# Kernel tuning notes

Measured on AMD Instinct MI355X. Metric: run time of the kernel, lower is better.

Reference implementation:

```python
import jax, jax.numpy as jnp
import numpy as np

B, S, D, HID, H, VOCAB, DFF = 4, 2048, 512, 512, 8, 32000, 2048
DK = HID // H   # per-head Q/K dim
DV = D // H     # per-head V dim


def sinusoidal_pe(L, d):
    pos = jnp.arange(L, dtype=jnp.float32)[:, None]
    i = jnp.arange(d, dtype=jnp.float32)[None, :]
    ang = pos / jnp.power(jnp.float32(10000.0), i / d)
    return jnp.where(jnp.arange(d)[None, :] % 2 == 0, jnp.sin(ang), jnp.cos(ang))  # [L, d]


def layer_norm(x, gamma, beta, eps=1e-5):
    mu = jnp.mean(x, axis=-1, keepdims=True)
    var = jnp.mean((x - mu) ** 2, axis=-1, keepdims=True)
    return (x - mu) * jax.lax.rsqrt(var + eps) * gamma + beta


def setup_inputs() -> dict:
    key = jax.random.key(0)
    ks = jax.random.split(key, 24)
    n = lambda k, shape, fan: jax.random.normal(k, shape, dtype=jnp.float32) / np.sqrt(fan)
    inp = {
        'x': jax.random.randint(ks[0], (B, S), 0, VOCAB),
        'emb': n(ks[1], (VOCAB, D), D),
        'WfQ': n(ks[2], (D, HID), D), 'bfQ': jnp.zeros((HID,), jnp.float32),
        'WfK': n(ks[3], (D, HID), D), 'bfK': jnp.zeros((HID,), jnp.float32),
        'WfV': n(ks[4], (D, D), D),   'bfV': jnp.zeros((D,), jnp.float32),
        'WQ': n(ks[5], (H, HID, DK), HID), 'bQ': jnp.zeros((H, DK), jnp.float32),
        'WK': n(ks[6], (H, HID, DK), HID), 'bK': jnp.zeros((H, DK), jnp.float32),
        'WV': n(ks[7], (H, D, DV), D),     'bV': jnp.zeros((H, DV), jnp.float32),
        'Wo': n(ks[8], (D, D), D),   'bo': jnp.zeros((D,), jnp.float32),
        'W1': n(ks[9], (D, DFF), D), 'b1': jnp.zeros((DFF,), jnp.float32),
        'W2': n(ks[10], (DFF, D), DFF), 'b2': jnp.zeros((D,), jnp.float32),
        'gamma': jnp.ones((D,), jnp.float32), 'beta': jnp.zeros((D,), jnp.float32),
    }
    return inp


def reference(x, emb, WfQ, bfQ, WfK, bfK, WfV, bfV, WQ, bQ, WK, bK, WV, bV,
              Wo, bo, W1, b1, W2, b2, gamma, beta):
    z = emb[x] + sinusoidal_pe(x.shape[1], D)[None]            # [B,S,D]
    Q = z @ WfQ + bfQ                                           # [B,S,HID]
    K = z @ WfK + bfK
    V = z @ WfV + bfV                                           # [B,S,D]
    # per-head projections (batched equivalent of the per-head Linear loop)
    Qh = jnp.einsum('bsd,hdk->bhsk', Q, WQ) + bQ[None, :, None, :]  # [B,H,S,DK]
    Kh = jnp.einsum('bsd,hdk->bhsk', K, WK) + bK[None, :, None, :]
    Vh = jnp.einsum('bsd,hdv->bhsv', V, WV) + bV[None, :, None, :]  # [B,H,S,DV]
    scores = jnp.einsum('bhqk,bhsk->bhqs', Qh, Kh) / np.sqrt(DK)    # [B,H,S,S]
    attn = jax.nn.softmax(scores, axis=-1)
    heads = jnp.einsum('bhqs,bhsv->bhqv', attn, Vh)                 # [B,H,S,DV]
    concat = heads.transpose(0, 2, 1, 3).reshape(x.shape[0], x.shape[1], D)
    attn_out = concat @ Wo + bo
    a = layer_norm(attn_out + z, gamma, beta)
    ffn = jax.nn.relu(a @ W1 + b1) @ W2 + b2
    out = layer_norm(ffn + a, gamma, beta)   # same (shared) LayerNorm params, as in source
    return jax.nn.relu(out)
```

## Files before the change

### kernel.cpp

```cpp
#include <hip/hip_runtime.h>
#include <math.h>

typedef __bf16 bf16;
typedef __bf16 bf16x8 __attribute__((ext_vector_type(8)));
typedef __bf16 bf16x4 __attribute__((ext_vector_type(4)));
typedef _Float16 f16;
typedef _Float16 f16x8 __attribute__((ext_vector_type(8)));
typedef _Float16 f16x4 __attribute__((ext_vector_type(4)));
typedef _Float16 f16x2 __attribute__((ext_vector_type(2)));
typedef __fp16 h16x2 __attribute__((ext_vector_type(2)));
typedef float f32x4 __attribute__((ext_vector_type(4)));
typedef unsigned int u32;

#define S_LEN 2048
#define QSCALE 0.18033688011112042f

#if __has_builtin(__builtin_amdgcn_exp2f)
#define EXP2(x) __builtin_amdgcn_exp2f(x)
#else
#define EXP2(x) exp2f(x)
#endif

__device__ __forceinline__ void gload_lds16(const void* g, void* l) {
  __builtin_amdgcn_global_load_lds((const __attribute__((address_space(1))) u32*)g,
                                   (__attribute__((address_space(3))) u32*)l, 16, 0, 0);
}

__global__ __launch_bounds__(256) void embed_pe(const int* __restrict__ x,
    const float* __restrict__ emb, bf16* __restrict__ zb)
{
  const int row = blockIdx.x;
  const int s = row & (S_LEN - 1);
  const int tok = x[row];
  const float* e = emb + (size_t)tok * 512;
  bf16* zbr = zb + (size_t)row * 512;
  for (int i = threadIdx.x; i < 512; i += 256) {
    float invf = __expf((float)i * (-9.210340371976184f / 512.0f));
    float ang = (float)s * invf;
    float pe = (i & 1) ? __cosf(ang) : __sinf(ang);
    zbr[i] = (bf16)(e[i] + pe);
  }
}

__global__ __launch_bounds__(256) void conv_t(
    const float* __restrict__ Wo, const float* __restrict__ W1, const float* __restrict__ W2,
    const float* __restrict__ WQ, const float* __restrict__ WK, const float* __restrict__ WV,
    const float* __restrict__ WfQ, const float* __restrict__ WfK, const float* __restrict__ WfV,
    bf16* __restrict__ wot, bf16* __restrict__ w1t, bf16* __restrict__ w2t,
    bf16* __restrict__ wqt, bf16* __restrict__ wkt, bf16* __restrict__ wvt,
    bf16* __restrict__ wfqp, bf16* __restrict__ wfkp, bf16* __restrict__ wfvp)
{
  __shared__ float T[64][65];
  const int y = blockIdx.y, x = blockIdx.x;
  if (y >= 6) {
    int g = x * 256 + threadIdx.x;
    const float* in = y == 6 ? WfQ : (y == 7 ? WfK : WfV);
    bf16* outp = y == 6 ? wfqp : (y == 7 ? wfkp : wfvp);
    float4 v = *(const float4*)(in + (size_t)g * 4);
    bf16x4 o = {(bf16)v.x, (bf16)v.y, (bf16)v.z, (bf16)v.w};
    *(bf16x4*)(outp + (size_t)g * 4) = o;
    return;
  }
  const int tx = threadIdx.x & 63, ty = threadIdx.x >> 6;
  const float* src; bf16* dst;
  int src_cols, dst_cols; float scale = 1.f;
  if (y == 0) {
    if (x >= 64) return;
    int kt = x & 7, nt = x >> 3;
    src = Wo + (size_t)(kt * 64) * 512 + nt * 64; src_cols = 512;
    dst = wot + (size_t)(nt * 64) * 512 + kt * 64; dst_cols = 512;
  } else if (y == 1) {
    int kt = x & 7, nt = x >> 3;
    src = W1 + (size_t)(kt * 64) * 2048 + nt * 64; src_cols = 2048;
    dst = w1t + (size_t)(nt * 64) * 512 + kt * 64; dst_cols = 512;
  } else if (y == 2) {
    int kt = x & 31, nt = x >> 5;
    src = W2 + (size_t)(kt * 64) * 512 + nt * 64; src_cols = 512;
    dst = w2t + (size_t)(nt * 64) * 2048 + kt * 64; dst_cols = 2048;
  } else {
    if (x >= 64) return;
    const float* W = y == 3 ? WQ : (y == 4 ? WK : WV);
    bf16* o = y == 3 ? wqt : (y == 4 ? wkt : wvt);
    if (y == 3) scale = QSCALE;
    int h = x >> 3, rt = x & 7;
    src = W + (size_t)(h * 512 + rt * 64) * 64; src_cols = 64;
    dst = o + (size_t)(h * 64) * 512 + rt * 64; dst_cols = 512;
  }
  #pragma unroll
  for (int i = 0; i < 16; i++) {
    int rr = i * 4 + ty;
    T[rr][tx] = src[(size_t)rr * src_cols + tx];
  }
  __syncthreads();
  #pragma unroll
  for (int i = 0; i < 16; i++) {
    int rr = i * 4 + ty;
    dst[(size_t)rr * dst_cols + tx] = (bf16)(T[tx][rr] * scale);
  }
}

__global__ __launch_bounds__(256) void bias_comb(
    const float* __restrict__ bfQ, const float* __restrict__ bfK, const float* __restrict__ bfV,
    const float* __restrict__ WQ, const float* __restrict__ WK, const float* __restrict__ WV,
    const float* __restrict__ bQ, const float* __restrict__ bK, const float* __restrict__ bV,
    float* __restrict__ bc)
{
  int n = blockIdx.x * 4 + (threadIdx.x >> 6);
  int lane = threadIdx.x & 63;
  int z = n >> 9, hk = n & 511, h = hk >> 6, k = hk & 63;
  const float* bf = z == 0 ? bfQ : (z == 1 ? bfK : bfV);
  const float* W  = z == 0 ? WQ  : (z == 1 ? WK  : WV);
  const float* bH = z == 0 ? bQ  : (z == 1 ? bK  : bV);
  float s = 0.f;
  for (int e = lane; e < 512; e += 64)
    s += bf[e] * W[((size_t)h * 512 + e) * 64 + k];
  #pragma unroll
  for (int m = 1; m < 64; m <<= 1) s += __shfl_xor(s, m, 64);
  if (lane == 0) {
    float v = s + bH[h * 64 + k];
    if (z == 0) v *= QSCALE;
    bc[n] = v;
  }
}

__global__ __launch_bounds__(256) void gemm_comb(
    const bf16* __restrict__ wqt, const bf16* __restrict__ wkt, const bf16* __restrict__ wvt,
    const bf16* __restrict__ wfqp, const bf16* __restrict__ wfkp, const bf16* __restrict__ wfvp,
    bf16* __restrict__ wc)
{
  __shared__ bf16 As[128 * 32];
  __shared__ bf16 Bs[64 * 32];
  const int z = blockIdx.z;
  const bf16* A  = z == 0 ? wqt : (z == 1 ? wkt : wvt);
  const bf16* Bt = z == 0 ? wfqp : (z == 1 ? wfkp : wfvp);
  bf16* outb = wc + (size_t)z * 262144;
  const int tid = threadIdx.x;
  const int wave = tid >> 6, lane = tid & 63, quad = lane >> 4, l16 = lane & 15;
  const int row0 = blockIdx.x * 128, col0 = blockIdx.y * 64;
  const int wm = wave >> 1, wn = wave & 1;
  f32x4 acc[4][2] = {};

  for (int kk = 0; kk < 512; kk += 32) {
    __syncthreads();
    #pragma unroll
    for (int r = 0; r < 2; r++) {
      int c = r * 256 + tid;
      gload_lds16(A + (size_t)(row0 + (c >> 2)) * 512 + kk + (c & 3) * 8, As + c * 8);
    }
    gload_lds16(Bt + (size_t)(col0 + (tid >> 2)) * 512 + kk + (tid & 3) * 8, Bs + tid * 8);
    __syncthreads();
    bf16x8 af[4], bfr[2];
    #pragma unroll
    for (int i = 0; i < 4; i++)
      af[i] = *(const bf16x8*)(As + (wm * 64 + i * 16 + l16) * 32 + quad * 8);
    #pragma unroll
    for (int i = 0; i < 2; i++)
      bfr[i] = *(const bf16x8*)(Bs + (wn * 32 + i * 16 + l16) * 32 + quad * 8);
    #pragma unroll
    for (int mt = 0; mt < 4; mt++)
      #pragma unroll
      for (int nt = 0; nt < 2; nt++)
        acc[mt][nt] = __builtin_amdgcn_mfma_f32_16x16x32_bf16(af[mt], bfr[nt], acc[mt][nt], 0, 0, 0);
  }
  #pragma unroll
  for (int nt = 0; nt < 2; nt++) {
    int col = col0 + wn * 32 + nt * 16 + l16;
    #pragma unroll
    for (int mt = 0; mt < 4; mt++) {
      int rowb = row0 + wm * 64 + mt * 16 + quad * 4;
      #pragma unroll
      for (int i = 0; i < 4; i++)
        outb[(size_t)(rowb + i) * 512 + col] = (bf16)acc[mt][nt][i];
    }
  }
}

#define GEMM_CORE(A_, Bt_, K_, KK0_, ITERS_)                                            \
  bf16x8 ar0, ar1, br0, br1;                                                            \
  const int c0 = tid, c1 = 256 + tid;                                                   \
  const size_t aoff0 = (size_t)(row0 + (c0 >> 2)) * (K_) + (c0 & 3) * 8;                \
  const size_t aoff1 = (size_t)(row0 + (c1 >> 2)) * (K_) + (c1 & 3) * 8;                \
  const size_t boff0 = (size_t)(col0 + (c0 >> 2)) * (K_) + (c0 & 3) * 8;                \
  const size_t boff1 = (size_t)(col0 + (c1 >> 2)) * (K_) + (c1 & 3) * 8;                \
  ar0 = *(const bf16x8*)((A_) + aoff0 + (KK0_));                                        \
  ar1 = *(const bf16x8*)((A_) + aoff1 + (KK0_));                                        \
  br0 = *(const bf16x8*)((Bt_) + boff0 + (KK0_));                                       \
  br1 = *(const bf16x8*)((Bt_) + boff1 + (KK0_));                                       \
  for (int it = 0; it < (ITERS_); it++) {                                               \
    bf16* AsB = As[it & 1];                                                             \
    bf16* BsB = Bs[it & 1];                                                             \
    *(bf16x8*)(AsB + c0 * 8) = ar0;                                                     \
    *(bf16x8*)(AsB + c1 * 8) = ar1;                                                     \
    *(bf16x8*)(BsB + c0 * 8) = br0;                                                     \
    *(bf16x8*)(BsB + c1 * 8) = br1;                                                     \
    __syncthreads();                                                                    \
    if (it + 1 < (ITERS_)) {                                                            \
      int kk = (KK0_) + (it + 1) * 32;                                                  \
      ar0 = *(const bf16x8*)((A_) + aoff0 + kk);                                        \
      ar1 = *(const bf16x8*)((A_) + aoff1 + kk);                                        \
      br0 = *(const bf16x8*)((Bt_) + boff0 + kk);                                      \
      br1 = *(const bf16x8*)((Bt_) + boff1 + kk);                                      \
    }                                                                                   \
    bf16x8 af[4], bfr[4];                                                               \
    _Pragma("unroll")                                                                   \
    for (int i = 0; i < 4; i++)                                                         \
      af[i] = *(const bf16x8*)(AsB + (wm * 64 + i * 16 + l16) * 32 + quad * 8);         \
    _Pragma("unroll")                                                                   \
    for (int i = 0; i < 4; i++)                                                         \
      bfr[i] = *(const bf16x8*)(BsB + (wn * 64 + i * 16 + l16) * 32 + quad * 8);        \
    _Pragma("unroll")                                                                   \
    for (int mt = 0; mt < 4; mt++)                                                      \
      _Pragma("unroll")                                                                 \
      for (int nt = 0; nt < 4; nt++)                                                    \
        acc[mt][nt] = __builtin_amdgcn_mfma_f32_16x16x32_bf16(af[mt], bfr[nt], acc[mt][nt], 0, 0, 0); \
  }

__global__ __launch_bounds__(256) void gemm_bt(
    const bf16* __restrict__ A, const bf16* __restrict__ Bt,
    const float* __restrict__ bias, bf16* __restrict__ outb,
    int M, int N, int K, int relu)
{
  __shared__ bf16 As[2][4096];
  __shared__ bf16 Bs[2][4096];
  const int tid = threadIdx.x;
  const int wave = tid >> 6, lane = tid & 63, quad = lane >> 4, l16 = lane & 15;
  const int row0 = blockIdx.x * 128, col0 = blockIdx.y * 128;
  const int wm = wave >> 1, wn = wave & 1;
  f32x4 acc[4][4] = {};
  GEMM_CORE(A, Bt, K, 0, K / 32)

  #pragma unroll
  for (int nt = 0; nt < 4; nt++) {
    int col = col0 + wn * 64 + nt * 16 + l16;
    float bv = bias[col];
    #pragma unroll
    for (int mt = 0; mt < 4; mt++) {
      int rowb = row0 + wm * 64 + mt * 16 + quad * 4;
      #pragma unroll
      for (int i = 0; i < 4; i++) {
        float v = acc[mt][nt][i] + bv;
        if (relu) v = fmaxf(v, 0.f);
        outb[(size_t)(rowb + i) * N + col] = (bf16)v;
      }
    }
  }
}

__global__ __launch_bounds__(256) void gemm_qkv(
    const bf16* __restrict__ A, const bf16* __restrict__ Bt,
    const float* __restrict__ bias, f16* __restrict__ qk, f16* __restrict__ Vt)
{
  __shared__ bf16 As[2][4096];
  __shared__ bf16 Bs[2][4096];
  const int tid = threadIdx.x;
  const int wave = tid >> 6, lane = tid & 63, quad = lane >> 4, l16 = lane & 15;
  const int row0 = blockIdx.x * 128, col0 = blockIdx.y * 128;
  const int wm = wave >> 1, wn = wave & 1;
  f32x4 acc[4][4] = {};
  GEMM_CORE(A, Bt, 512, 0, 16)

  #pragma unroll
  for (int nt = 0; nt < 4; nt++) {
    int col = col0 + wn * 64 + nt * 16 + l16;
    float bv = bias[col];
    if (col < 1024) {
      #pragma unroll
      for (int mt = 0; mt < 4; mt++) {
        int rowb = row0 + wm * 64 + mt * 16 + quad * 4;
        #pragma unroll
        for (int i = 0; i < 4; i++)
          qk[(size_t)(rowb + i) * 1024 + col] = (f16)(acc[mt][nt][i] + bv);
      }
    } else {
      int h = (col - 1024) >> 6, dv = col & 63;
      #pragma unroll
      for (int mt = 0; mt < 4; mt++) {
        int rowb = row0 + wm * 64 + mt * 16 + quad * 4;
        int b = rowb >> 11, s = rowb & 2047;
        f16x4 vv;
        #pragma unroll
        for (int i = 0; i < 4; i++) vv[i] = (f16)(acc[mt][nt][i] + bv);
        *(f16x4*)(Vt + ((size_t)((b * 8 + h) * 64 + dv)) * 2048 + s) = vv;
      }
    }
  }
}

__global__ __launch_bounds__(256) void gemm_part(
    const bf16* __restrict__ A, const bf16* __restrict__ Bt,
    bf16* __restrict__ Pa, bf16* __restrict__ Pb, int N, int K, int Kh)
{
  __shared__ bf16 As[2][4096];
  __shared__ bf16 Bs[2][4096];
  const int tid = threadIdx.x;
  const int wave = tid >> 6, lane = tid & 63, quad = lane >> 4, l16 = lane & 15;
  const int row0 = blockIdx.x * 128, col0 = blockIdx.y * 128;
  const int wm = wave >> 1, wn = wave & 1;
  const int kk0 = blockIdx.z * Kh;
  bf16* P = blockIdx.z ? Pb : Pa;
  f32x4 acc[4][4] = {};
  GEMM_CORE(A, Bt, K, kk0, Kh / 32)

  #pragma unroll
  for (int nt = 0; nt < 4; nt++) {
    int col = col0 + wn * 64 + nt * 16 + l16;
    #pragma unroll
    for (int mt = 0; mt < 4; mt++) {
      int rowb = row0 + wm * 64 + mt * 16 + quad * 4;
      #pragma unroll
      for (int i = 0; i < 4; i++)
        P[(size_t)(rowb + i) * N + col] = (bf16)acc[mt][nt][i];
    }
  }
}

__global__ __launch_bounds__(256, 2) void flash_attn(
    const f16* __restrict__ qk, const f16* __restrict__ Vt,
    bf16* __restrict__ Op, float* __restrict__ Rp)
{
  __shared__ f16 Ks[2][4096];
  __shared__ f16 Vs[2][4096];
  const int bh = blockIdx.y, b = bh >> 3, h = bh & 7;
  const int q0 = blockIdx.x * 128;
  const int quarter = blockIdx.z;
  const int tid = threadIdx.x;
  const int wave = tid >> 6, lane = tid & 63, quad = lane >> 4, l16 = lane & 15;

  const f16* Qb = qk + ((size_t)b * S_LEN) * 1024 + h * 64;
  const f16* Kb = Qb + 512;
  const f16* Vtb = Vt + ((size_t)bh * 64) * 2048;
  const int key0 = quarter * 512;

  f16x8 qf[2][2];
  #pragma unroll
  for (int f = 0; f < 2; f++) {
    int qrow = q0 + wave * 32 + f * 16 + l16;
    #pragma unroll
    for (int kh = 0; kh < 2; kh++)
      qf[f][kh] = *(const f16x8*)(Qb + (size_t)qrow * 1024 + kh * 32 + quad * 8);
  }

  f32x4 O[2][4] = {};
  f32x4 Osum[2] = {};
  const f16x4 onesA = {(f16)1.f, (f16)1.f, (f16)1.f, (f16)1.f};
  const int swz = l16 & 7;

  f16x8 kreg[2], vreg[2];
  const int srow = tid >> 3, soff = tid & 7;
  const int srow1 = srow + 32;

  {
    int kb = key0;
    kreg[0] = *(const f16x8*)(Kb + (size_t)(kb + srow) * 1024 + soff * 8);
    vreg[0] = *(const f16x8*)(Vtb + (size_t)srow * 2048 + kb + soff * 8);
    kreg[1] = *(const f16x8*)(Kb + (size_t)(kb + srow1) * 1024 + soff * 8);
    vreg[1] = *(const f16x8*)(Vtb + (size_t)srow1 * 2048 + kb + soff * 8);
  }

  for (int c = 0; c < 8; c++) {
    f16* KsB = Ks[c & 1];
    f16* VsB = Vs[c & 1];
    *(f16x8*)(KsB + srow * 64 + ((soff ^ (srow & 7)) * 8)) = kreg[0];
    *(f16x8*)(VsB + srow * 64 + ((soff ^ (srow & 7)) * 8)) = vreg[0];
    *(f16x8*)(KsB + srow1 * 64 + ((soff ^ (srow1 & 7)) * 8)) = kreg[1];
    *(f16x8*)(VsB + srow1 * 64 + ((soff ^ (srow1 & 7)) * 8)) = vreg[1];
    __syncthreads();
    if (c < 7) {
      int kb = key0 + (c + 1) * 64;
      kreg[0] = *(const f16x8*)(Kb + (size_t)(kb + srow) * 1024 + soff * 8);
      vreg[0] = *(const f16x8*)(Vtb + (size_t)srow * 2048 + kb + soff * 8);
      kreg[1] = *(const f16x8*)(Kb + (size_t)(kb + srow1) * 1024 + soff * 8);
      vreg[1] = *(const f16x8*)(Vtb + (size_t)srow1 * 2048 + kb + soff * 8);
    }

    #pragma unroll
    for (int nt = 0; nt < 4; nt++) {
      const f16* kp = KsB + (nt * 16 + l16) * 64;
      f16x8 kf0 = *(const f16x8*)(kp + ((quad ^ swz) * 8));
      f16x8 kf1 = *(const f16x8*)(kp + (((4 + quad) ^ swz) * 8));
      f16x4 pf[2];
      f32x4 a0 = {}, a1 = {};
      __builtin_amdgcn_s_setprio(1);
      a0 = __builtin_amdgcn_mfma_f32_16x16x32_f16(kf0, qf[0][0], a0, 0, 0, 0);
      a0 = __builtin_amdgcn_mfma_f32_16x16x32_f16(kf1, qf[0][1], a0, 0, 0, 0);
      a1 = __builtin_amdgcn_mfma_f32_16x16x32_f16(kf0, qf[1][0], a1, 0, 0, 0);
      a1 = __builtin_amdgcn_mfma_f32_16x16x32_f16(kf1, qf[1][1], a1, 0, 0, 0);
      __builtin_amdgcn_s_setprio(0);
      #pragma unroll
      for (int f = 0; f < 2; f++) {
        const f32x4& a = f == 0 ? a0 : a1;
        float e0 = EXP2(a[0]);
        float e1 = EXP2(a[1]);
        float e2 = EXP2(a[2]);
        float e3 = EXP2(a[3]);
        h16x2 lo = __builtin_amdgcn_cvt_pkrtz(e0, e1);
        h16x2 hi = __builtin_amdgcn_cvt_pkrtz(e2, e3);
        f16x2 lo2 = __builtin_bit_cast(f16x2, lo);
        f16x2 hi2 = __builtin_bit_cast(f16x2, hi);
        pf[f] = __builtin_shufflevector(lo2, hi2, 0, 1, 2, 3);
        Osum[f] = __builtin_amdgcn_mfma_f32_16x16x16f16(onesA, pf[f], Osum[f], 0, 0, 0);
      }
      int vchunk = nt * 2 + (quad >> 1);
      __builtin_amdgcn_s_setprio(1);
      #pragma unroll
      for (int mt = 0; mt < 4; mt++) {
        const f16* vp = VsB + (mt * 16 + l16) * 64 + ((vchunk ^ swz) * 8) + (quad & 1) * 4;
        f16x4 vf = *(const f16x4*)vp;
        #pragma unroll
        for (int f = 0; f < 2; f++)
          O[f][mt] = __builtin_amdgcn_mfma_f32_16x16x16f16(vf, pf[f], O[f][mt], 0, 0, 0);
      }
      __builtin_amdgcn_s_setprio(0);
    }
  }

  #pragma unroll
  for (int f = 0; f < 2; f++) {
    bf16* ob = (f == 0 ? (bf16*)&Ks[0][0] : (bf16*)&Vs[0][0]) + wave * 1024;
    #pragma unroll
    for (int mt = 0; mt < 4; mt++) {
      bf16x4 w;
      #pragma unroll
      for (int i = 0; i < 4; i++) w[i] = (bf16)O[f][mt][i];
      int chunk = mt * 2 + (quad >> 1);
      *(bf16x4*)(ob + l16 * 64 + ((chunk ^ (l16 & 7)) << 3) + (quad & 1) * 4) = w;
    }
  }
  asm volatile("s_waitcnt lgkmcnt(0)" ::: "memory");
  const size_t obase = (size_t)(quarter * 32 + bh) * 2048;
  #pragma unroll
  for (int f = 0; f < 2; f++) {
    const bf16* ob = (f == 0 ? (const bf16*)&Ks[0][0] : (const bf16*)&Vs[0][0]) + wave * 1024;
    int row = lane >> 2, cc = (lane & 3) * 2;
    bf16x8 o0 = *(const bf16x8*)(ob + row * 64 + ((cc ^ (row & 7)) << 3));
    bf16x8 o1 = *(const bf16x8*)(ob + row * 64 + (((cc + 1) ^ (row & 7)) << 3));
    size_t g = (obase + q0 + wave * 32 + f * 16 + row) * 64 + (lane & 3) * 16;
    *(bf16x8*)(Op + g) = o0;
    *(bf16x8*)(Op + g + 8) = o1;
    if (quad == f)
      Rp[obase + q0 + wave * 32 + f * 16 + l16] = Osum[f][0];
  }
}

__global__ __launch_bounds__(256) void attn_merge(const bf16* __restrict__ Op,
    const float* __restrict__ Rp, bf16* __restrict__ concat)
{
  int t = blockIdx.x * 256 + threadIdx.x;
  int dv4 = t & 15, s = (t >> 4) & 2047, bh = t >> 15;
  int rb = bh * 2048 + s;
  float r = (Rp[rb] + Rp[65536 + rb]) + (Rp[131072 + rb] + Rp[196608 + rb]);
  float inv = 1.f / r;
  size_t ia = ((size_t)bh * 2048 + s) * 64 + dv4 * 4;
  bf16x4 p0 = *(const bf16x4*)(Op + ia);
  bf16x4 p1 = *(const bf16x4*)(Op + 4194304ull + ia);
  bf16x4 p2 = *(const bf16x4*)(Op + 8388608ull + ia);
  bf16x4 p3 = *(const bf16x4*)(Op + 12582912ull + ia);
  bf16x4 o;
  #pragma unroll
  for (int i = 0; i < 4; i++)
    o[i] = (bf16)((((float)p0[i] + (float)p1[i]) + ((float)p2[i] + (float)p3[i])) * inv);
  int b = bh >> 3, h = bh & 7;
  *(bf16x4*)(concat + ((size_t)(b * 2048 + s)) * 512 + h * 64 + dv4 * 4) = o;
}

__global__ __launch_bounds__(256) void ln_merge(const bf16* __restrict__ Pa,
    const bf16* __restrict__ Pb, const float* __restrict__ badd,
    const bf16* __restrict__ resid, const float* __restrict__ gamma,
    const float* __restrict__ beta, float* __restrict__ outf,
    bf16* __restrict__ outb, int relu)
{
  const int row = blockIdx.x * 4 + (threadIdx.x >> 6);
  const int lane = threadIdx.x & 63;
  const size_t base = (size_t)row * 512;
  const int e0 = lane * 8;
  bf16x8 pa = *(const bf16x8*)(Pa + base + e0);
  bf16x8 pb = *(const bf16x8*)(Pb + base + e0);
  bf16x8 rr = *(const bf16x8*)(resid + base + e0);
  float4 C0 = *(const float4*)(badd + e0);
  float4 C1 = *(const float4*)(badd + e0 + 4);
  float v[8];
  v[0] = (float)pa[0] + (float)pb[0] + (float)rr[0] + C0.x;
  v[1] = (float)pa[1] + (float)pb[1] + (float)rr[1] + C0.y;
  v[2] = (float)pa[2] + (float)pb[2] + (float)rr[2] + C0.z;
  v[3] = (float)pa[3] + (float)pb[3] + (float)rr[3] + C0.w;
  v[4] = (float)pa[4] + (float)pb[4] + (float)rr[4] + C1.x;
  v[5] = (float)pa[5] + (float)pb[5] + (float)rr[5] + C1.y;
  v[6] = (float)pa[6] + (float)pb[6] + (float)rr[6] + C1.z;
  v[7] = (float)pa[7] + (float)pb[7] + (float)rr[7] + C1.w;
  float s = 0.f;
  #pragma unroll
  for (int i = 0; i < 8; i++) s += v[i];
  #pragma unroll
  for (int m = 1; m < 64; m <<= 1) s += __shfl_xor(s, m, 64);
  float mu = s * (1.f / 512.f);
  float d[8], q = 0.f;
  #pragma unroll
  for (int i = 0; i < 8; i++) { d[i] = v[i] - mu; q += d[i] * d[i]; }
  #pragma unroll
  for (int m = 1; m < 64; m <<= 1) q += __shfl_xor(q, m, 64);
  float rsn = rsqrtf(q * (1.f / 512.f) + 1e-5f);
  float4 g0 = *(const float4*)(gamma + e0);
  float4 g1 = *(const float4*)(gamma + e0 + 4);
  float4 b0 = *(const float4*)(beta + e0);
  float4 b1 = *(const float4*)(beta + e0 + 4);
  float y[8];
  y[0] = d[0] * rsn * g0.x + b0.x; y[1] = d[1] * rsn * g0.y + b0.y;
  y[2] = d[2] * rsn * g0.z + b0.z; y[3] = d[3] * rsn * g0.w + b0.w;
  y[4] = d[4] * rsn * g1.x + b1.x; y[5] = d[5] * rsn * g1.y + b1.y;
  y[6] = d[6] * rsn * g1.z + b1.z; y[7] = d[7] * rsn * g1.w + b1.w;
  if (relu) {
    #pragma unroll
    for (int i = 0; i < 8; i++) y[i] = fmaxf(y[i], 0.f);
  }
  if (outf) {
    float4 o0 = {y[0], y[1], y[2], y[3]}, o1 = {y[4], y[5], y[6], y[7]};
    *(float4*)(outf + base + e0) = o0;
    *(float4*)(outf + base + e0 + 4) = o1;
  }
  if (outb) {
    bf16x8 ob;
    #pragma unroll
    for (int i = 0; i < 8; i++) ob[i] = (bf16)y[i];
    *(bf16x8*)(outb + base + e0) = ob;
  }
}

extern "C" void kernel_launch(void* const* d_in, const int* in_sizes, int n_in,
                              void* d_out, int out_size, void* d_ws, size_t ws_size,
                              hipStream_t stream)
{
  const int*   x    = (const int*)  d_in[0];
  const float* emb  = (const float*)d_in[1];
  const float* WfQ  = (const float*)d_in[2];
  const float* bfQv = (const float*)d_in[3];
  const float* WfK  = (const float*)d_in[4];
  const float* bfKv = (const float*)d_in[5];
  const float* WfV  = (const float*)d_in[6];
  const float* bfVv = (const float*)d_in[7];
  const float* WQ   = (const float*)d_in[8];
  const float* bQ   = (const float*)d_in[9];
  const float* WK   = (const float*)d_in[10];
  const float* bK   = (const float*)d_in[11];
  const float* WV   = (const float*)d_in[12];
  const float* bV   = (const float*)d_in[13];
  const float* Wo   = (const float*)d_in[14];
  const float* bo   = (const float*)d_in[15];
  const float* W1   = (const float*)d_in[16];
  const float* b1   = (const float*)d_in[17];
  const float* W2   = (const float*)d_in[18];
  const float* b2   = (const float*)d_in[19];
  const float* gamma= (const float*)d_in[20];
  const float* beta = (const float*)d_in[21];
  float* out = (float*)d_out;

  char* ws = (char*)d_ws;
  const size_t MB = 1024ull * 1024;
  bf16*  bz   = (bf16*) (ws);
  f16*   qkh  = (f16*)  (ws + 8 * MB);
  f16*   Vt   = (f16*)  (ws + 24 * MB);
  bf16*  Op   = (bf16*) (ws + 32 * MB);
  float* Rp   = (float*)(ws + 64 * MB);
  bf16*  concat = (bf16*)(ws + 66 * MB);
  bf16*  PaW  = (bf16*) (ws + 32 * MB);
  bf16*  PbW  = (bf16*) (ws + 40 * MB);
  bf16*  ffn1 = (bf16*) (ws + 8 * MB);
  bf16*  Pa2  = (bf16*) (ws + 40 * MB);
  bf16*  Pb2  = (bf16*) (ws + 48 * MB);
  char* wp = ws + 74 * MB;
  bf16* wfqp = (bf16*)(wp);
  bf16* wfkp = (bf16*)(wp + 512 * 1024);
  bf16* wfvp = (bf16*)(wp + 1024 * 1024);
  bf16* wqt  = (bf16*)(wp + 1536 * 1024);
  bf16* wkt  = (bf16*)(wp + 2048 * 1024);
  bf16* wvt  = (bf16*)(wp + 2560 * 1024);
  bf16* wc   = (bf16*)(wp + 3072 * 1024);
  bf16* wot  = (bf16*)(wp + 4608 * 1024);
  bf16* w1t  = (bf16*)(wp + 5120 * 1024);
  bf16* w2t  = (bf16*)(wp + 7168 * 1024);
  float* bc  = (float*)(wp + 9216 * 1024);

  conv_t<<<dim3(256, 9), 256, 0, stream>>>(Wo, W1, W2, WQ, WK, WV, WfQ, WfK, WfV,
                                           wot, w1t, w2t, wqt, wkt, wvt, wfqp, wfkp, wfvp);
  bias_comb<<<384, 256, 0, stream>>>(bfQv, bfKv, bfVv, WQ, WK, WV, bQ, bK, bV, bc);
  gemm_comb<<<dim3(4, 8, 3), 256, 0, stream>>>(wqt, wkt, wvt, wfqp, wfkp, wfvp, wc);

  embed_pe<<<8192, 256, 0, stream>>>(x, emb, bz);

  gemm_qkv<<<dim3(64, 12), 256, 0, stream>>>(bz, wc, bc, qkh, Vt);
  flash_attn<<<dim3(16, 32, 4), 256, 0, stream>>>(qkh, Vt, Op, Rp);
  attn_merge<<<4096, 256, 0, stream>>>(Op, Rp, concat);

  gemm_part<<<dim3(64, 4, 2), 256, 0, stream>>>(concat, wot, PaW, PbW, 512, 512, 256);
  ln_merge<<<2048, 256, 0, stream>>>(PaW, PbW, bo, bz, gamma, beta, nullptr, bz, 0);
  gemm_bt<<<dim3(64, 16), 256, 0, stream>>>(bz, w1t, b1, ffn1, 8192, 2048, 512, 1);
  gemm_part<<<dim3(64, 4, 2), 256, 0, stream>>>(ffn1, w2t, Pa2, Pb2, 512, 2048, 1024);
  ln_merge<<<2048, 256, 0, stream>>>(Pa2, Pb2, b2, bz, gamma, beta, out, nullptr, 1);
}
```

Measured before the change: 323.9 us.

## Fuse attention split-merge into Wo GEMM and bias combine into weight conversion

Removes the attn_merge kernel by having a new gemm_wo kernel read the four split-key partial outputs and row sums directly, normalizing them while staging A tiles into LDS. This avoids writing and re-reading the concat buffer. The bias_comb launch is also folded into conv_t as an extra grid row, saving one launch. In exchange, gemm_wo reads the A operand four times per tile (once per partial) and uses a simpler register-prefetch pipeline than the shared GEMM core. The workspace offsets for PaW/PbW are moved so they no longer overlap Op.

```diff
diff --git a/kernel.cpp b/kernel.cpp
--- a/kernel.cpp
+++ b/kernel.cpp
@@ -46,13 +46,36 @@
     const float* __restrict__ Wo, const float* __restrict__ W1, const float* __restrict__ W2,
     const float* __restrict__ WQ, const float* __restrict__ WK, const float* __restrict__ WV,
     const float* __restrict__ WfQ, const float* __restrict__ WfK, const float* __restrict__ WfV,
+    const float* __restrict__ bfQ, const float* __restrict__ bfK, const float* __restrict__ bfV,
+    const float* __restrict__ bQ, const float* __restrict__ bK, const float* __restrict__ bV,
     bf16* __restrict__ wot, bf16* __restrict__ w1t, bf16* __restrict__ w2t,
     bf16* __restrict__ wqt, bf16* __restrict__ wkt, bf16* __restrict__ wvt,
-    bf16* __restrict__ wfqp, bf16* __restrict__ wfkp, bf16* __restrict__ wfvp)
+    bf16* __restrict__ wfqp, bf16* __restrict__ wfkp, bf16* __restrict__ wfvp,
+    float* __restrict__ bc)
 {
   __shared__ float T[64][65];
   const int y = blockIdx.y, x = blockIdx.x;
+  if (y == 9) {
+    int n = x * 4 + ((int)threadIdx.x >> 6);
+    int lane = threadIdx.x & 63;
+    int z = n >> 9, hk = n & 511, h = hk >> 6, k = hk & 63;
+    const float* bf = z == 0 ? bfQ : (z == 1 ? bfK : bfV);
+    const float* W  = z == 0 ? WQ  : (z == 1 ? WK  : WV);
+    const float* bH = z == 0 ? bQ  : (z == 1 ? bK  : bV);
+    float s = 0.f;
+    for (int e = lane; e < 512; e += 64)
+      s += bf[e] * W[((size_t)h * 512 + e) * 64 + k];
+    #pragma unroll
+    for (int m = 1; m < 64; m <<= 1) s += __shfl_xor(s, m, 64);
+    if (lane == 0) {
+      float v = s + bH[h * 64 + k];
+      if (z == 0) v *= QSCALE;
+      bc[n] = v;
+    }
+    return;
+  }
   if (y >= 6) {
+    if (x >= 256) return;
     int g = x * 256 + threadIdx.x;
     const float* in = y == 6 ? WfQ : (y == 7 ? WfK : WfV);
     bf16* outp = y == 6 ? wfqp : (y == 7 ? wfkp : wfvp);
@@ -70,10 +93,12 @@
     src = Wo + (size_t)(kt * 64) * 512 + nt * 64; src_cols = 512;
     dst = wot + (size_t)(nt * 64) * 512 + kt * 64; dst_cols = 512;
   } else if (y == 1) {
+    if (x >= 256) return;
     int kt = x & 7, nt = x >> 3;
     src = W1 + (size_t)(kt * 64) * 2048 + nt * 64; src_cols = 2048;
     dst = w1t + (size_t)(nt * 64) * 512 + kt * 64; dst_cols = 512;
   } else if (y == 2) {
+    if (x >= 256) return;
     int kt = x & 31, nt = x >> 5;
     src = W2 + (size_t)(kt * 64) * 512 + nt * 64; src_cols = 512;
     dst = w2t + (size_t)(nt * 64) * 2048 + kt * 64; dst_cols = 2048;
@@ -96,30 +121,6 @@
   for (int i = 0; i < 16; i++) {
     int rr = i * 4 + ty;
     dst[(size_t)rr * dst_cols + tx] = (bf16)(T[tx][rr] * scale);
-  }
-}
-
-__global__ __launch_bounds__(256) void bias_comb(
-    const float* __restrict__ bfQ, const float* __restrict__ bfK, const float* __restrict__ bfV,
-    const float* __restrict__ WQ, const float* __restrict__ WK, const float* __restrict__ WV,
-    const float* __restrict__ bQ, const float* __restrict__ bK, const float* __restrict__ bV,
-    float* __restrict__ bc)
-{
-  int n = blockIdx.x * 4 + (threadIdx.x >> 6);
-  int lane = threadIdx.x & 63;
-  int z = n >> 9, hk = n & 511, h = hk >> 6, k = hk & 63;
-  const float* bf = z == 0 ? bfQ : (z == 1 ? bfK : bfV);
-  const float* W  = z == 0 ? WQ  : (z == 1 ? WK  : WV);
-  const float* bH = z == 0 ? bQ  : (z == 1 ? bK  : bV);
-  float s = 0.f;
-  for (int e = lane; e < 512; e += 64)
-    s += bf[e] * W[((size_t)h * 512 + e) * 64 + k];
-  #pragma unroll
-  for (int m = 1; m < 64; m <<= 1) s += __shfl_xor(s, m, 64);
-  if (lane == 0) {
-    float v = s + bH[h * 64 + k];
-    if (z == 0) v *= QSCALE;
-    bc[n] = v;
   }
 }
 
@@ -314,6 +315,114 @@
   }
 }
 
+__global__ __launch_bounds__(256) void gemm_wo(
+    const bf16* __restrict__ Op, const float* __restrict__ Rp,
+    const bf16* __restrict__ Bt, bf16* __restrict__ Pa, bf16* __restrict__ Pb)
+{
+  __shared__ bf16 As[2][4096];
+  __shared__ bf16 Bs[2][4096];
+  const int tid = threadIdx.x;
+  const int wave = tid >> 6, lane = tid & 63, quad = lane >> 4, l16 = lane & 15;
+  const int row0 = blockIdx.x * 128, col0 = blockIdx.y * 128;
+  const int wm = wave >> 1, wn = wave & 1;
+  const int kk0 = blockIdx.z * 256;
+  bf16* P = blockIdx.z ? Pb : Pa;
+  f32x4 acc[4][4] = {};
+
+  const int c0 = tid, c1 = 256 + tid;
+  const int r0 = row0 + (c0 >> 2), r1 = r0 + 64;
+  const int b0 = r0 >> 11, s0 = r0 & 2047;
+  const int b1 = r1 >> 11, s1 = r1 & 2047;
+  const int ccol = (c0 & 3) * 8;
+  const int h0 = kk0 >> 6;
+  const size_t boff0 = (size_t)(col0 + (c0 >> 2)) * 512 + ccol;
+  const size_t boff1 = (size_t)(col0 + 64 + (c0 >> 2)) * 512 + ccol;
+
+  float inv0[4], inv1[4];
+  #pragma unroll
+  for (int hh = 0; hh < 4; hh++) {
+    int hg = h0 + hh;
+    int ra = (b0 * 8 + hg) * 2048 + s0;
+    float r = (Rp[ra] + Rp[65536 + ra]) + (Rp[131072 + ra] + Rp[196608 + ra]);
+    inv0[hh] = 1.f / r;
+    int rb = (b1 * 8 + hg) * 2048 + s1;
+    r = (Rp[rb] + Rp[65536 + rb]) + (Rp[131072 + rb] + Rp[196608 + rb]);
+    inv1[hh] = 1.f / r;
+  }
+
+  bf16x8 p0q[4], p1q[4], br0, br1;
+  {
+    int hg = h0, dv = ccol;
+    size_t ia0 = ((size_t)(b0 * 8 + hg) * 2048 + s0) * 64 + dv;
+    size_t ia1 = ((size_t)(b1 * 8 + hg) * 2048 + s1) * 64 + dv;
+    #pragma unroll
+    for (int q = 0; q < 4; q++) {
+      p0q[q] = *(const bf16x8*)(Op + q * 4194304ull + ia0);
+      p1q[q] = *(const bf16x8*)(Op + q * 4194304ull + ia1);
+    }
+    br0 = *(const bf16x8*)(Bt + boff0 + kk0);
+    br1 = *(const bf16x8*)(Bt + boff1 + kk0);
+  }
+
+  for (int it = 0; it < 8; it++) {
+    bf16* AsB = As[it & 1];
+    bf16* BsB = Bs[it & 1];
+    const float iv0 = inv0[it >> 1], iv1 = inv1[it >> 1];
+    bf16x8 a0v, a1v;
+    #pragma unroll
+    for (int i = 0; i < 8; i++) {
+      float v0 = ((float)p0q[0][i] + (float)p0q[1][i]) + ((float)p0q[2][i] + (float)p0q[3][i]);
+      float v1 = ((float)p1q[0][i] + (float)p1q[1][i]) + ((float)p1q[2][i] + (float)p1q[3][i]);
+      a0v[i] = (bf16)(v0 * iv0);
+      a1v[i] = (bf16)(v1 * iv1);
+    }
+    *(bf16x8*)(AsB + c0 * 8) = a0v;
+    *(bf16x8*)(AsB + c1 * 8) = a1v;
+    *(bf16x8*)(BsB + c0 * 8) = br0;
+    *(bf16x8*)(BsB + c1 * 8) = br1;
+    __syncthreads();
+    if (it < 7) {
+      int itn = it + 1;
+      int kk = kk0 + itn * 32;
+      int hg = h0 + (itn >> 1);
+      int dv = (itn & 1) * 32 + ccol;
+      size_t ia0 = ((size_t)(b0 * 8 + hg) * 2048 + s0) * 64 + dv;
+      size_t ia1 = ((size_t)(b1 * 8 + hg) * 2048 + s1) * 64 + dv;
+      #pragma unroll
+      for (int q = 0; q < 4; q++) {
+        p0q[q] = *(const bf16x8*)(Op + q * 4194304ull + ia0);
+        p1q[q] = *(const bf16x8*)(Op + q * 4194304ull + ia1);
+      }
+      br0 = *(const bf16x8*)(Bt + boff0 + kk);
+      br1 = *(const bf16x8*)(Bt + boff1 + kk);
+    }
+    bf16x8 af[4], bfr[4];
+    #pragma unroll
+    for (int i = 0; i < 4; i++)
+      af[i] = *(const bf16x8*)(AsB + (wm * 64 + i * 16 + l16) * 32 + quad * 8);
+    #pragma unroll
+    for (int i = 0; i < 4; i++)
+      bfr[i] = *(const bf16x8*)(BsB + (wn * 64 + i * 16 + l16) * 32 + quad * 8);
+    #pragma unroll
+    for (int mt = 0; mt < 4; mt++)
+      #pragma unroll
+      for (int nt = 0; nt < 4; nt++)
+        acc[mt][nt] = __builtin_amdgcn_mfma_f32_16x16x32_bf16(af[mt], bfr[nt], acc[mt][nt], 0, 0, 0);
+  }
+
+  #pragma unroll
+  for (int nt = 0; nt < 4; nt++) {
+    int col = col0 + wn * 64 + nt * 16 + l16;
+    #pragma unroll
+    for (int mt = 0; mt < 4; mt++) {
+      int rowb = row0 + wm * 64 + mt * 16 + quad * 4;
+      #pragma unroll
+      for (int i = 0; i < 4; i++)
+        P[(size_t)(rowb + i) * 512 + col] = (bf16)acc[mt][nt][i];
+    }
+  }
+}
+
 __global__ __launch_bounds__(256, 2) void flash_attn(
     const f16* __restrict__ qk, const f16* __restrict__ Vt,
     bf16* __restrict__ Op, float* __restrict__ Rp)
@@ -440,27 +549,6 @@
     if (quad == f)
       Rp[obase + q0 + wave * 32 + f * 16 + l16] = Osum[f][0];
   }
-}
-
-__global__ __launch_bounds__(256) void attn_merge(const bf16* __restrict__ Op,
-    const float* __restrict__ Rp, bf16* __restrict__ concat)
-{
-  int t = blockIdx.x * 256 + threadIdx.x;
-  int dv4 = t & 15, s = (t >> 4) & 2047, bh = t >> 15;
-  int rb = bh * 2048 + s;
-  float r = (Rp[rb] + Rp[65536 + rb]) + (Rp[131072 + rb] + Rp[196608 + rb]);
-  float inv = 1.f / r;
-  size_t ia = ((size_t)bh * 2048 + s) * 64 + dv4 * 4;
-  bf16x4 p0 = *(const bf16x4*)(Op + ia);
-  bf16x4 p1 = *(const bf16x4*)(Op + 4194304ull + ia);
-  bf16x4 p2 = *(const bf16x4*)(Op + 8388608ull + ia);
-  bf16x4 p3 = *(const bf16x4*)(Op + 12582912ull + ia);
-  bf16x4 o;
-  #pragma unroll
-  for (int i = 0; i < 4; i++)
-    o[i] = (bf16)((((float)p0[i] + (float)p1[i]) + ((float)p2[i] + (float)p3[i])) * inv);
-  int b = bh >> 3, h = bh & 7;
-  *(bf16x4*)(concat + ((size_t)(b * 2048 + s)) * 512 + h * 64 + dv4 * 4) = o;
 }
 
 __global__ __launch_bounds__(256) void ln_merge(const bf16* __restrict__ Pa,
@@ -560,9 +648,8 @@
   f16*   Vt   = (f16*)  (ws + 24 * MB);
   bf16*  Op   = (bf16*) (ws + 32 * MB);
   float* Rp   = (float*)(ws + 64 * MB);
-  bf16*  concat = (bf16*)(ws + 66 * MB);
-  bf16*  PaW  = (bf16*) (ws + 32 * MB);
-  bf16*  PbW  = (bf16*) (ws + 40 * MB);
+  bf16*  PaW  = (bf16*) (ws + 8 * MB);
+  bf16*  PbW  = (bf16*) (ws + 16 * MB);
   bf16*  ffn1 = (bf16*) (ws + 8 * MB);
   bf16*  Pa2  = (bf16*) (ws + 40 * MB);
   bf16*  Pb2  = (bf16*) (ws + 48 * MB);
@@ -579,18 +666,18 @@
   bf16* w2t  = (bf16*)(wp + 7168 * 1024);
   float* bc  = (float*)(wp + 9216 * 1024);
 
-  conv_t<<<dim3(256, 9), 256, 0, stream>>>(Wo, W1, W2, WQ, WK, WV, WfQ, WfK, WfV,
-                                           wot, w1t, w2t, wqt, wkt, wvt, wfqp, wfkp, wfvp);
-  bias_comb<<<384, 256, 0, stream>>>(bfQv, bfKv, bfVv, WQ, WK, WV, bQ, bK, bV, bc);
+  conv_t<<<dim3(384, 10), 256, 0, stream>>>(Wo, W1, W2, WQ, WK, WV, WfQ, WfK, WfV,
+                                            bfQv, bfKv, bfVv, bQ, bK, bV,
+                                            wot, w1t, w2t, wqt, wkt, wvt,
+                                            wfqp, wfkp, wfvp, bc);
   gemm_comb<<<dim3(4, 8, 3), 256, 0, stream>>>(wqt, wkt, wvt, wfqp, wfkp, wfvp, wc);
 
   embed_pe<<<8192, 256, 0, stream>>>(x, emb, bz);
 
   gemm_qkv<<<dim3(64, 12), 256, 0, stream>>>(bz, wc, bc, qkh, Vt);
   flash_attn<<<dim3(16, 32, 4), 256, 0, stream>>>(qkh, Vt, Op, Rp);
-  attn_merge<<<4096, 256, 0, stream>>>(Op, Rp, concat);
-
-  gemm_part<<<dim3(64, 4, 2), 256, 0, stream>>>(concat, wot, PaW, PbW, 512, 512, 256);
+
+  gemm_wo<<<dim3(64, 4, 2), 256, 0, stream>>>(Op, Rp, wot, PaW, PbW);
   ln_merge<<<2048, 256, 0, stream>>>(PaW, PbW, bo, bz, gamma, beta, nullptr, bz, 0);
   gemm_bt<<<dim3(64, 16), 256, 0, stream>>>(bz, w1t, b1, ffn1, 8192, 2048, 512, 1);
   gemm_part<<<dim3(64, 4, 2), 256, 0, stream>>>(ffn1, w2t, Pa2, Pb2, 512, 2048, 1024);
```

Measured after the change: 315.0 us. 1.03x faster.
